# Kernel optimization log

Measured on AMD Instinct MI355X. Metric: run time of the kernel, lower is better.

The kernel has to match this reference:

```python
import jax, jax.numpy as jnp
import numpy as np

B, N, D, H, L = 16, 512, 256, 8, 4
DK = D // H
EPS_LN = 1e-6
EPS_ADJ = 1e-6
NEG_INF = -1e12
LAM_ATT, LAM_DIST, LAM_ADJ = 0.3, 0.3, 0.4
SLOPE = 0.1  # leaky_relu_slope


def setup_inputs() -> dict:
    key = jax.random.key(0)
    ks = jax.random.split(key, 24)
    s = 1.0 / np.sqrt(D)
    w = lambda k: jax.random.normal(k, (L, D, D), jnp.float32) * s
    b = lambda k: jax.random.normal(k, (L, D), jnp.float32) * 0.01
    return {
        "x": jax.random.normal(ks[0], (B, N, D), jnp.float32),
        "mask": jax.random.randint(ks[1], (B, N), 0, 2, jnp.int32),
        "adj_matrix": jax.random.uniform(ks[2], (B, N, N), jnp.float32),
        "distance_matrix": jax.random.uniform(ks[3], (B, N, N), jnp.float32) * 10.0,
        "edges_att": jnp.zeros((1,), jnp.float32),  # unused (use_edge_features=False)
        "Wq": w(ks[4]), "bq": b(ks[5]),
        "Wk": w(ks[6]), "bk": b(ks[7]),
        "Wv": w(ks[8]), "bv": b(ks[9]),
        "Wo": w(ks[10]), "bo": b(ks[11]),
        "Wf1": w(ks[12]), "bf1": b(ks[13]),
        "Wf2": w(ks[14]), "bf2": b(ks[15]),
        "ln1_a": jnp.ones((L, D), jnp.float32), "ln1_b": jnp.zeros((L, D), jnp.float32),
        "ln2_a": jnp.ones((L, D), jnp.float32), "ln2_b": jnp.zeros((L, D), jnp.float32),
        "lnf_a": jnp.ones((D,), jnp.float32), "lnf_b": jnp.zeros((D,), jnp.float32),
    }


def _layernorm(x, a, b):
    # torch LayerNorm here uses unbiased std and divides by (std + eps)
    m = x.mean(-1, keepdims=True)
    s = jnp.std(x, axis=-1, ddof=1, keepdims=True)
    return a * (x - m) / (s + EPS_LN) + b


def reference(x, mask, adj_matrix, distance_matrix, edges_att,
              Wq, bq, Wk, bk, Wv, bv, Wo, bo, Wf1, bf1, Wf2, bf2,
              ln1_a, ln1_b, ln2_a, ln2_b, lnf_a, lnf_b):
    maskk = (mask != 0)[:, None, :]                      # [B,1,N] key mask
    # distance kernel: softmax(-dist) with masked keys -> weight 0
    p_dist = jax.nn.softmax(jnp.where(maskk, -distance_matrix, -jnp.inf), axis=-1)  # [B,N,N]
    # row-normalized adjacency
    p_adj = adj_matrix / (adj_matrix.sum(-1, keepdims=True) + EPS_ADJ)              # [B,N,N]
    mk4 = maskk[:, :, None, :]                           # [B,1,1,N]
    inv_sqrt_dk = 1.0 / np.sqrt(DK)

    for i in range(L):
        # --- self-attention sublayer (pre-norm residual) ---
        h_in = _layernorm(x, ln1_a[i], ln1_b[i])
        q = (h_in @ Wq[i] + bq[i]).reshape(B, N, H, DK).transpose(0, 2, 1, 3)
        k = (h_in @ Wk[i] + bk[i]).reshape(B, N, H, DK).transpose(0, 2, 1, 3)
        v = (h_in @ Wv[i] + bv[i]).reshape(B, N, H, DK).transpose(0, 2, 1, 3)
        scores = jnp.einsum('bhqd,bhkd->bhqk', q, k) * inv_sqrt_dk
        p_attn = jax.nn.softmax(jnp.where(mk4, scores, NEG_INF), axis=-1)
        # three-way fused weighting over [B,H,N,N]
        p = LAM_ATT * p_attn + LAM_DIST * p_dist[:, None] + LAM_ADJ * p_adj[:, None]
        att = jnp.einsum('bhqk,bhkd->bhqd', p, v).transpose(0, 2, 1, 3).reshape(B, N, D)
        x = x + (att @ Wo[i] + bo[i])
        # --- FFN sublayer (pre-norm residual), N_dense=2 with leaky_relu ---
        h2 = _layernorm(x, ln2_a[i], ln2_b[i])
        h2 = jax.nn.leaky_relu(h2 @ Wf1[i] + bf1[i], negative_slope=SLOPE)
        h2 = jax.nn.leaky_relu(h2 @ Wf2[i] + bf2[i], negative_slope=SLOPE)
        x = x + h2

    return _layernorm(x, lnf_a, lnf_b)
```

## Files before the change

### kernel.cpp

```cpp
#include <hip/hip_runtime.h>
#include <hip/hip_bf16.h>
#include <math.h>

constexpr int kB  = 16;
constexpr int kN  = 512;
constexpr int kD  = 256;
constexpr int kH  = 8;
constexpr int kDK = 32;
constexpr int kL  = 4;

using bf16 = __hip_bfloat16;
using short8 = __attribute__((ext_vector_type(8))) short;
using floatx4 = __attribute__((ext_vector_type(4))) float;

__device__ __forceinline__ float fast_exp2(float x) {
#if __has_builtin(__builtin_amdgcn_exp2f)
    return __builtin_amdgcn_exp2f(x);
#else
    return __expf(x * 0.69314718055994531f);
#endif
}

__device__ __forceinline__ float bfs2f(short s) {
    unsigned u = ((unsigned)(unsigned short)s) << 16;
    return __uint_as_float(u);
}

__device__ __forceinline__ void gl2lds16(const bf16* g, bf16* s) {
    __builtin_amdgcn_global_load_lds(
        (const __attribute__((address_space(1))) void*)g,
        (__attribute__((address_space(3))) void*)s, 16, 0, 0);
}

__device__ __forceinline__ int swzA(int row, int inrow_byte) {
    return row * 512 + (inrow_byte ^ ((row & 7) << 4));
}

__device__ __forceinline__ float blockReduceSum(float v, float* sh) {
    #pragma unroll
    for (int o = 32; o > 0; o >>= 1) v += __shfl_down(v, o, 64);
    int lane = threadIdx.x & 63, w = threadIdx.x >> 6;
    __syncthreads();
    if (lane == 0) sh[w] = v;
    __syncthreads();
    return sh[0] + sh[1] + sh[2] + sh[3];
}

__device__ __forceinline__ float blockReduceMax(float v, float* sh) {
    #pragma unroll
    for (int o = 32; o > 0; o >>= 1) v = fmaxf(v, __shfl_down(v, o, 64));
    int lane = threadIdx.x & 63, w = threadIdx.x >> 6;
    __syncthreads();
    if (lane == 0) sh[w] = v;
    __syncthreads();
    return fmaxf(fmaxf(sh[0], sh[1]), fmaxf(sh[2], sh[3]));
}

__global__ __launch_bounds__(256) void wconv_kernel(const float* __restrict__ Wq,
                                                    const float* __restrict__ Wk,
                                                    const float* __restrict__ Wv,
                                                    const float* __restrict__ Wo,
                                                    const float* __restrict__ Wf1,
                                                    const float* __restrict__ Wf2,
                                                    bf16* __restrict__ wqkv,
                                                    bf16* __restrict__ wo,
                                                    bf16* __restrict__ wf1,
                                                    bf16* __restrict__ wf2) {
    __shared__ float tile[32][33];
    int bid = blockIdx.x;
    int mat = bid >> 6;
    int t6 = bid & 63;
    int tr = t6 >> 3, tc = t6 & 7;
    int layer = mat / 6, slot = mat % 6;
    const float* src =
        slot == 0 ? Wq : slot == 1 ? Wk : slot == 2 ? Wv :
        slot == 3 ? Wo : slot == 4 ? Wf1 : Wf2;
    src += (size_t)layer * kD * kD;
    bf16* dst;
    if (slot < 3) dst = wqkv + ((size_t)layer * 768 + slot * 256) * kD;
    else dst = (slot == 3 ? wo : slot == 4 ? wf1 : wf2) + (size_t)layer * kD * kD;
    int t = threadIdx.x;
    int r = t >> 5, c = t & 31;
    #pragma unroll
    for (int i = 0; i < 4; i++)
        tile[r + i * 8][c] = src[(size_t)(tr * 32 + r + i * 8) * kD + tc * 32 + c];
    __syncthreads();
    #pragma unroll
    for (int i = 0; i < 4; i++)
        dst[(size_t)(tc * 32 + r + i * 8) * kD + tr * 32 + c] = bf16(tile[c][r + i * 8]);
}

__global__ __launch_bounds__(256) void bcat_kernel(const float* __restrict__ bq,
                                                   const float* __restrict__ bk,
                                                   const float* __restrict__ bv,
                                                   float* __restrict__ bcat) {
    int idx = blockIdx.x * 256 + threadIdx.x;
    int layer = idx / 768, j = idx % 768;
    const float* s = j < 256 ? bq : j < 512 ? bk : bv;
    bcat[idx] = s[layer * 256 + (j & 255)];
}

__global__ __launch_bounds__(256) void pc_kernel(const float* __restrict__ adj,
                                                 const float* __restrict__ dist,
                                                 const int* __restrict__ mask,
                                                 bf16* __restrict__ pcb) {
    __shared__ float sh[4];
    int row = blockIdx.x;
    int b = row >> 9;
    int t = threadIdx.x;
    const float* dr = dist + (size_t)row * kN;
    const float* ar = adj + (size_t)row * kN;
    const int* mr = mask + b * kN;
    float d0 = dr[t], d1 = dr[t + 256];
    float a0 = ar[t], a1 = ar[t + 256];
    int m0 = mr[t], m1 = mr[t + 256];
    const float kLog2e = 1.4426950408889634f;
    float s0 = m0 ? -d0 * kLog2e : -INFINITY;
    float s1 = m1 ? -d1 * kLog2e : -INFINITY;
    float mx = blockReduceMax(fmaxf(s0, s1), sh);
    float e0 = fast_exp2(s0 - mx);
    float e1 = fast_exp2(s1 - mx);
    float sum  = blockReduceSum(e0 + e1, sh);
    float asum = blockReduceSum(a0 + a1, sh);
    float w_d = 0.3f / sum;
    float w_a = 0.4f / (asum + 1e-6f);
    bf16* pr = pcb + (size_t)row * kN;
    pr[t]       = bf16(e0 * w_d + a0 * w_a);
    pr[t + 256] = bf16(e1 * w_d + a1 * w_a);
}

__global__ __launch_bounds__(256) void ln_kernel(const float* __restrict__ x,
                                                 const float* __restrict__ ga,
                                                 const float* __restrict__ gb,
                                                 bf16* __restrict__ y) {
    __shared__ float sh[4];
    int row = blockIdx.x, t = threadIdx.x;
    float v = x[(size_t)row * kD + t];
    float m = blockReduceSum(v, sh) * (1.0f / kD);
    float dd = v - m;
    float var = blockReduceSum(dd * dd, sh) * (1.0f / (kD - 1));
    float s = sqrtf(var);
    y[(size_t)row * kD + t] = bf16(ga[t] * dd / (s + 1e-6f) + gb[t]);
}

__global__ __launch_bounds__(256) void gemm_qkv(const bf16* __restrict__ A,
                                                const bf16* __restrict__ Wt,
                                                const float* __restrict__ bias,
                                                bf16* __restrict__ Cv) {
    __shared__ __align__(16) bf16 As[2][128][32];
    __shared__ __align__(16) bf16 Bs[2][64][32];
    int t = threadIdx.x;
    int m0 = blockIdx.x * 128, n0 = blockIdx.y * 64;
    int lane = t & 63, w = t >> 6, g = lane >> 4, li = lane & 15;
    int sr = lane >> 2;
    int sc = (lane & 3) * 8;

    const bf16* aSrc0 = A + (size_t)(m0 + w * 32 + sr) * kD + sc;
    const bf16* aSrc1 = aSrc0 + (size_t)16 * kD;
    const bf16* bSrc  = Wt + (size_t)(n0 + w * 16 + sr) * kD + sc;

    floatx4 zero = {0.f, 0.f, 0.f, 0.f};
    floatx4 acc[2][4];
    #pragma unroll
    for (int i = 0; i < 2; i++)
        #pragma unroll
        for (int j = 0; j < 4; j++) acc[i][j] = zero;

    auto stage = [&](int buf, int k0) {
        gl2lds16(aSrc0 + k0, &As[buf][w * 32][0]);
        gl2lds16(aSrc1 + k0, &As[buf][w * 32 + 16][0]);
        gl2lds16(bSrc  + k0, &Bs[buf][w * 16][0]);
    };

    stage(0, 0);
    __syncthreads();

    #pragma unroll
    for (int ks = 0; ks < 8; ks++) {
        const int cur = ks & 1;
        if (ks < 7) stage(cur ^ 1, (ks + 1) * 32);
        short8 af0 = *(const short8*)&As[cur][w * 32 + li][g * 8];
        short8 af1 = *(const short8*)&As[cur][w * 32 + 16 + li][g * 8];
        #pragma unroll
        for (int ct = 0; ct < 4; ct++) {
            short8 bfr = *(const short8*)&Bs[cur][ct * 16 + li][g * 8];
            acc[0][ct] = __builtin_amdgcn_mfma_f32_16x16x32_bf16(af0, bfr, acc[0][ct], 0, 0, 0);
            acc[1][ct] = __builtin_amdgcn_mfma_f32_16x16x32_bf16(af1, bfr, acc[1][ct], 0, 0, 0);
        }
        if (ks < 7) __syncthreads();
    }

    #pragma unroll
    for (int rt = 0; rt < 2; rt++) {
        #pragma unroll
        for (int ct = 0; ct < 4; ct++) {
            #pragma unroll
            for (int rr = 0; rr < 4; rr++) {
                int m = m0 + w * 32 + rt * 16 + g * 4 + rr;
                int n = n0 + ct * 16 + li;
                float v = acc[rt][ct][rr] + bias[n];
                int j = n >> 8, nn = n & 255;
                int b = m >> 9, nr = m & 511;
                int hh = nn >> 5, dk = nn & 31;
                Cv[(size_t)j * (kB * kN * kD) +
                   (((size_t)(b * kH + hh)) * kN + nr) * kDK + dk] = bf16(v);
            }
        }
    }
}

__global__ __launch_bounds__(256, 2) void attn_mfma(const bf16* __restrict__ qb,
                                                    const bf16* __restrict__ kb,
                                                    const bf16* __restrict__ vb,
                                                    const bf16* __restrict__ pcb,
                                                    const int* __restrict__ mask,
                                                    bf16* __restrict__ att) {
    __shared__ __align__(16) bf16 Vf[16 * 2 * 64 * 8];
    __shared__ __align__(16) bf16 Pbuf[4][16][136];

    int blk = blockIdx.x;
    int qt = blk & 7;
    int bh = blk >> 3;
    int b = bh >> 3;
    int h = bh & 7;
    int t = threadIdx.x;
    int lane = t & 63, w = t >> 6;
    int g = lane >> 4, li = lane & 15;

    {
        const float4* vsrc4 = (const float4*)(vb + (size_t)bh * kN * kDK);
        #pragma unroll
        for (int it = 0; it < 8; it++) {
            int idx = t + it * 256;
            float4 raw = vsrc4[idx];
            union { float4 f; bf16 hh[8]; } u; u.f = raw;
            int f0 = idx * 8;
            int n = f0 >> 5, dk0 = f0 & 31;
            int kt = n >> 5, j = n & 7, gsl = (n >> 3) & 3;
            #pragma unroll
            for (int e = 0; e < 8; e++) {
                int dk = dk0 + e;
                int dt = dk >> 4;
                int lsl = (gsl << 4) | (dk & 15);
                Vf[((((kt << 1) | dt) << 6) | lsl) * 8 + j] = u.hh[e];
            }
        }
    }
    __syncthreads();

    const bf16* qrow = qb + ((size_t)bh * kN + qt * 64 + w * 16 + li) * kDK + g * 8;
    short8 aQ = *(const short8*)qrow;
    const bf16* kbase = kb + (size_t)bh * kN * kDK;
    const int* mb = mask + b * kN;
    unsigned mbits = 0;
    #pragma unroll
    for (int tt = 0; tt < 32; tt++)
        mbits |= (unsigned)(mb[tt * 16 + li] != 0) << tt;

    floatx4 s[32];
    floatx4 zero = {0.f, 0.f, 0.f, 0.f};
    #pragma unroll
    for (int tt = 0; tt < 32; tt++) {
        short8 bK = *(const short8*)(kbase + (size_t)(tt * 16 + li) * kDK + g * 8);
        s[tt] = __builtin_amdgcn_mfma_f32_16x16x32_bf16(aQ, bK, zero, 0, 0, 0);
    }

    const float scale = 0.17677669529663689f * 1.4426950408889634f;
    #pragma unroll
    for (int tt = 0; tt < 32; tt++) {
        bool mm = (mbits >> tt) & 1;
        #pragma unroll
        for (int r = 0; r < 4; r++)
            s[tt][r] = mm ? s[tt][r] * scale : -1e12f;
    }

    #pragma unroll
    for (int r = 0; r < 4; r++) {
        float mx = s[0][r];
        #pragma unroll
        for (int tt = 1; tt < 32; tt++) mx = fmaxf(mx, s[tt][r]);
        #pragma unroll
        for (int o = 1; o < 16; o <<= 1) mx = fmaxf(mx, __shfl_xor(mx, o, 64));
        float sum = 0.f;
        #pragma unroll
        for (int tt = 0; tt < 32; tt++) {
            float e = fast_exp2(s[tt][r] - mx);
            s[tt][r] = e;
            sum += e;
        }
        #pragma unroll
        for (int o = 1; o < 16; o <<= 1) sum += __shfl_xor(sum, o, 64);
        float inv = 0.3f / sum;
        #pragma unroll
        for (int tt = 0; tt < 32; tt++) s[tt][r] *= inv;
    }

    {
        const short* pcq = (const short*)(pcb + ((size_t)b * kN + qt * 64 + w * 16) * kN);
        #pragma unroll
        for (int tt = 0; tt < 32; tt++) {
            #pragma unroll
            for (int r = 0; r < 4; r++)
                s[tt][r] += bfs2f(pcq[(size_t)(g * 4 + r) * kN + tt * 16 + li]);
        }
    }

    bf16* pb = &Pbuf[w][0][0];
    floatx4 accA0 = zero, accA1 = zero;
    #pragma unroll
    for (int c = 0; c < 4; c++) {
        #pragma unroll
        for (int ttl = 0; ttl < 8; ttl++) {
            int tt = c * 8 + ttl;
            int kcol = ttl * 16 + li;
            #pragma unroll
            for (int r = 0; r < 4; r++)
                pb[(g * 4 + r) * 136 + kcol] = bf16(s[tt][r]);
        }
        #pragma unroll
        for (int k2 = 0; k2 < 4; k2++) {
            int ktile = c * 4 + k2;
            short8 aP  = *(const short8*)(pb + li * 136 + k2 * 32 + g * 8);
            short8 bV0 = *(const short8*)(&Vf[((ktile * 2 + 0) * 64 + lane) * 8]);
            short8 bV1 = *(const short8*)(&Vf[((ktile * 2 + 1) * 64 + lane) * 8]);
            accA0 = __builtin_amdgcn_mfma_f32_16x16x32_bf16(aP, bV0, accA0, 0, 0, 0);
            accA1 = __builtin_amdgcn_mfma_f32_16x16x32_bf16(aP, bV1, accA1, 0, 0, 0);
        }
    }

    #pragma unroll
    for (int r = 0; r < 4; r++) {
        size_t row = (size_t)b * kN + qt * 64 + w * 16 + g * 4 + r;
        bf16* arow = att + row * kD + h * kDK;
        arow[li]      = bf16(accA0[r]);
        arow[16 + li] = bf16(accA1[r]);
    }
}

__device__ __forceinline__ void gemm_phase32(const char* asb, const bf16* __restrict__ Wt,
                                             bf16 (*Bs)[256][32],
                                             int w, int lane, int g, int li,
                                             floatx4 acc[2][4]) {
    auto stageB = [&](int buf, int k0) {
        #pragma unroll
        for (int c = 0; c < 4; c++) {
            int row = w * 64 + c * 16;
            gl2lds16(Wt + (size_t)(row + (lane >> 2)) * kD + k0 + (lane & 3) * 8,
                     &Bs[buf][row][0]);
        }
    };
    stageB(0, 0);
    __syncthreads();
    #pragma unroll
    for (int ks = 0; ks < 8; ks++) {
        const int cur = ks & 1;
        if (ks < 7) stageB(cur ^ 1, (ks + 1) * 32);
        short8 af0 = *(const short8*)(asb + swzA(li,      (ks * 4 + g) << 4));
        short8 af1 = *(const short8*)(asb + swzA(li + 16, (ks * 4 + g) << 4));
        #pragma unroll
        for (int ct = 0; ct < 4; ct++) {
            short8 bfr = *(const short8*)&Bs[cur][w * 64 + ct * 16 + li][g * 8];
            acc[0][ct] = __builtin_amdgcn_mfma_f32_16x16x32_bf16(af0, bfr, acc[0][ct], 0, 0, 0);
            acc[1][ct] = __builtin_amdgcn_mfma_f32_16x16x32_bf16(af1, bfr, acc[1][ct], 0, 0, 0);
        }
        if (ks < 7) __syncthreads();
    }
}

__device__ __forceinline__ void row_ln_stats(floatx4 xv[2][4],
                                             float (*psumS)[32], float (*psqS)[32],
                                             int w, int g, int li,
                                             float outMean[2][4], float outInv[2][4]) {
    #pragma unroll
    for (int rt = 0; rt < 2; rt++) {
        #pragma unroll
        for (int rr = 0; rr < 4; rr++) {
            float s4 = 0.f, q4 = 0.f;
            #pragma unroll
            for (int ct = 0; ct < 4; ct++) {
                float v = xv[rt][ct][rr];
                s4 += v;
                q4 += v * v;
            }
            #pragma unroll
            for (int o = 1; o < 16; o <<= 1) {
                s4 += __shfl_xor(s4, o, 64);
                q4 += __shfl_xor(q4, o, 64);
            }
            int row = rt * 16 + g * 4 + rr;
            if (li == 0) { psumS[w][row] = s4; psqS[w][row] = q4; }
        }
    }
    __syncthreads();
    #pragma unroll
    for (int rt = 0; rt < 2; rt++) {
        #pragma unroll
        for (int rr = 0; rr < 4; rr++) {
            int row = rt * 16 + g * 4 + rr;
            float s  = psumS[0][row] + psumS[1][row] + psumS[2][row] + psumS[3][row];
            float ss = psqS[0][row]  + psqS[1][row]  + psqS[2][row]  + psqS[3][row];
            float mean = s * (1.0f / kD);
            float var = (ss - (float)kD * mean * mean) * (1.0f / (kD - 1));
            outMean[rt][rr] = mean;
            outInv[rt][rr] = 1.0f / (sqrtf(var) + 1e-6f);
        }
    }
}

template <bool LAST>
__global__ __launch_bounds__(256) void block_tail(const bf16* __restrict__ A,
                                                  const bf16* __restrict__ Wot,
                                                  const float* __restrict__ bo,
                                                  const float* __restrict__ resid,
                                                  const bf16* __restrict__ W1t,
                                                  const float* __restrict__ b1,
                                                  const bf16* __restrict__ W2t,
                                                  const float* __restrict__ b2,
                                                  const float* __restrict__ ln2a,
                                                  const float* __restrict__ ln2b,
                                                  const float* __restrict__ lnna,
                                                  const float* __restrict__ lnnb,
                                                  float* __restrict__ xcOut,
                                                  bf16* __restrict__ hOut,
                                                  float* __restrict__ fOut) {
    __shared__ __align__(16) bf16 As[32][256];
    __shared__ __align__(16) bf16 As2[32][256];
    __shared__ __align__(16) bf16 Bs[2][256][32];
    __shared__ float psumS[4][32], psqS[4][32];

    int t = threadIdx.x;
    int m0 = blockIdx.x * 32;
    int lane = t & 63, w = t >> 6, g = lane >> 4, li = lane & 15;

    {
        int r = t >> 3;
        int cbase = (t & 7) * 4;
        const bf16* src = A + (size_t)(m0 + r) * kD;
        char* asb = (char*)&As[0][0];
        #pragma unroll
        for (int c = 0; c < 4; c++) {
            int chunk = cbase + c;
            short8 v = *(const short8*)(src + chunk * 8);
            *(short8*)(asb + swzA(r, chunk << 4)) = v;
        }
    }

    floatx4 zero = {0.f, 0.f, 0.f, 0.f};
    floatx4 acc[2][4];
    #pragma unroll
    for (int i = 0; i < 2; i++)
        #pragma unroll
        for (int j = 0; j < 4; j++) acc[i][j] = zero;

    gemm_phase32((const char*)&As[0][0], Wot, Bs, w, lane, g, li, acc);

    floatx4 xs[2][4];
    #pragma unroll
    for (int rt = 0; rt < 2; rt++) {
        #pragma unroll
        for (int ct = 0; ct < 4; ct++) {
            #pragma unroll
            for (int rr = 0; rr < 4; rr++) {
                int m = m0 + rt * 16 + g * 4 + rr;
                int n = w * 64 + ct * 16 + li;
                float xv = resid[(size_t)m * kD + n] + acc[rt][ct][rr] + bo[n];
                xs[rt][ct][rr] = xv;
                acc[rt][ct][rr] = xv;
            }
        }
    }

    float mean[2][4], inv[2][4];
    row_ln_stats(acc, psumS, psqS, w, g, li, mean, inv);
    {
        char* asb = (char*)&As[0][0];
        #pragma unroll
        for (int rt = 0; rt < 2; rt++) {
            #pragma unroll
            for (int ct = 0; ct < 4; ct++) {
                #pragma unroll
                for (int rr = 0; rr < 4; rr++) {
                    int row = rt * 16 + g * 4 + rr;
                    int col = w * 64 + ct * 16 + li;
                    float y = ln2a[col] * (xs[rt][ct][rr] - mean[rt][rr]) * inv[rt][rr] + ln2b[col];
                    *(bf16*)(asb + swzA(row, col * 2)) = bf16(y);
                }
            }
        }
    }
    __syncthreads();

    #pragma unroll
    for (int i = 0; i < 2; i++)
        #pragma unroll
        for (int j = 0; j < 4; j++) acc[i][j] = zero;

    gemm_phase32((const char*)&As[0][0], W1t, Bs, w, lane, g, li, acc);

    {
        char* as2b = (char*)&As2[0][0];
        #pragma unroll
        for (int rt = 0; rt < 2; rt++) {
            #pragma unroll
            for (int ct = 0; ct < 4; ct++) {
                #pragma unroll
                for (int rr = 0; rr < 4; rr++) {
                    int row = rt * 16 + g * 4 + rr;
                    int col = w * 64 + ct * 16 + li;
                    float v = acc[rt][ct][rr] + b1[col];
                    v = v > 0.f ? v : 0.1f * v;
                    *(bf16*)(as2b + swzA(row, col * 2)) = bf16(v);
                }
            }
        }
    }
    __syncthreads();

    #pragma unroll
    for (int i = 0; i < 2; i++)
        #pragma unroll
        for (int j = 0; j < 4; j++) acc[i][j] = zero;

    gemm_phase32((const char*)&As2[0][0], W2t, Bs, w, lane, g, li, acc);

    #pragma unroll
    for (int rt = 0; rt < 2; rt++) {
        #pragma unroll
        for (int ct = 0; ct < 4; ct++) {
            #pragma unroll
            for (int rr = 0; rr < 4; rr++) {
                int m = m0 + rt * 16 + g * 4 + rr;
                int n = w * 64 + ct * 16 + li;
                float v = acc[rt][ct][rr] + b2[n];
                v = v > 0.f ? v : 0.1f * v;
                float xv = xs[rt][ct][rr] + v;
                if (!LAST) xcOut[(size_t)m * kD + n] = xv;
                acc[rt][ct][rr] = xv;
            }
        }
    }

    row_ln_stats(acc, psumS, psqS, w, g, li, mean, inv);

    #pragma unroll
    for (int rt = 0; rt < 2; rt++) {
        #pragma unroll
        for (int ct = 0; ct < 4; ct++) {
            #pragma unroll
            for (int rr = 0; rr < 4; rr++) {
                int m = m0 + rt * 16 + g * 4 + rr;
                int n = w * 64 + ct * 16 + li;
                float y = lnna[n] * (acc[rt][ct][rr] - mean[rt][rr]) * inv[rt][rr] + lnnb[n];
                if (LAST) fOut[(size_t)m * kD + n] = y;
                else      hOut[(size_t)m * kD + n] = bf16(y);
            }
        }
    }
}

extern "C" void kernel_launch(void* const* d_in, const int* in_sizes, int n_in,
                              void* d_out, int out_size, void* d_ws, size_t ws_size,
                              hipStream_t stream) {
    const float* x    = (const float*)d_in[0];
    const int*   mask = (const int*)d_in[1];
    const float* adj  = (const float*)d_in[2];
    const float* dist = (const float*)d_in[3];
    const float* Wq = (const float*)d_in[5];  const float* bq = (const float*)d_in[6];
    const float* Wk = (const float*)d_in[7];  const float* bk = (const float*)d_in[8];
    const float* Wv = (const float*)d_in[9];  const float* bv = (const float*)d_in[10];
    const float* Wo = (const float*)d_in[11]; const float* bo = (const float*)d_in[12];
    const float* Wf1 = (const float*)d_in[13]; const float* bf1 = (const float*)d_in[14];
    const float* Wf2 = (const float*)d_in[15]; const float* bf2 = (const float*)d_in[16];
    const float* ln1a = (const float*)d_in[17]; const float* ln1b = (const float*)d_in[18];
    const float* ln2a = (const float*)d_in[19]; const float* ln2b = (const float*)d_in[20];
    const float* lnfa = (const float*)d_in[21]; const float* lnfb = (const float*)d_in[22];

    const size_t rows = (size_t)kB * kN;
    const size_t actN = rows * kD;

    char* wsb = (char*)d_ws;
    bf16*  pcb   = (bf16*)wsb;  wsb += (size_t)kB * kN * kN * sizeof(bf16);
    float* xc    = (float*)wsb; wsb += actN * sizeof(float);
    bf16*  h     = (bf16*)wsb;  wsb += actN * sizeof(bf16);
    bf16*  attb  = (bf16*)wsb;  wsb += actN * sizeof(bf16);
    bf16*  qkvb  = (bf16*)wsb;  wsb += 3 * actN * sizeof(bf16);
    bf16*  wqkv  = (bf16*)wsb;  wsb += (size_t)kL * 768 * kD * sizeof(bf16);
    bf16*  wo_t  = (bf16*)wsb;  wsb += (size_t)kL * kD * kD * sizeof(bf16);
    bf16*  wf1_t = (bf16*)wsb;  wsb += (size_t)kL * kD * kD * sizeof(bf16);
    bf16*  wf2_t = (bf16*)wsb;  wsb += (size_t)kL * kD * kD * sizeof(bf16);
    float* bcat  = (float*)wsb; wsb += (size_t)kL * 768 * sizeof(float);

    wconv_kernel<<<24 * 64, 256, 0, stream>>>(Wq, Wk, Wv, Wo, Wf1, Wf2, wqkv, wo_t, wf1_t, wf2_t);
    bcat_kernel<<<kL * 768 / 256, 256, 0, stream>>>(bq, bk, bv, bcat);
    pc_kernel<<<kB * kN, 256, 0, stream>>>(adj, dist, mask, pcb);
    ln_kernel<<<rows, 256, 0, stream>>>(x, ln1a, ln1b, h);

    dim3 gQKV(64, 12);
    const int g32 = rows / 32;
    for (int i = 0; i < kL; i++) {
        const size_t bOff = (size_t)i * kD;
        const size_t wOff = (size_t)i * kD * kD;
        const float* xin = (i == 0) ? x : xc;
        gemm_qkv<<<gQKV, 256, 0, stream>>>(h, wqkv + (size_t)i * 768 * kD,
                                           bcat + (size_t)i * 768, qkvb);
        attn_mfma<<<kB * kH * (kN / 64), 256, 0, stream>>>(qkvb, qkvb + actN,
                                                           qkvb + 2 * actN,
                                                           pcb, mask, attb);
        if (i < kL - 1) {
            block_tail<false><<<g32, 256, 0, stream>>>(
                attb, wo_t + wOff, bo + bOff, xin,
                wf1_t + wOff, bf1 + bOff, wf2_t + wOff, bf2 + bOff,
                ln2a + bOff, ln2b + bOff,
                ln1a + (size_t)(i + 1) * kD, ln1b + (size_t)(i + 1) * kD,
                xc, h, nullptr);
        } else {
            block_tail<true><<<g32, 256, 0, stream>>>(
                attb, wo_t + wOff, bo + bOff, xin,
                wf1_t + wOff, bf1 + bOff, wf2_t + wOff, bf2 + bOff,
                ln2a + bOff, ln2b + bOff, lnfa, lnfb,
                nullptr, nullptr, (float*)d_out);
        }
    }
}
```

Measured before the change: 386.6 us.

## Merge prep kernels into one launch and process two query tiles per attention block

Folds the weight transpose/convert, bias concat, distance/adjacency precompute and first layernorm into a single prep kernel that dispatches on block index, saving three launches. The attention kernel now has each block handle two 64-row query tiles. That halves the grid and reuses the shared-memory V staging and mask bits across both tiles. The cost is fewer blocks (512) to fill the GPU and a longer serial chain per block, which can hurt latency hiding. The merged prep kernel also carries the larger shared tile for every block.

```diff
diff --git a/kernel.cpp b/kernel.cpp
--- a/kernel.cpp
+++ b/kernel.cpp
@@ -56,91 +56,89 @@
     return fmaxf(fmaxf(sh[0], sh[1]), fmaxf(sh[2], sh[3]));
 }
 
-__global__ __launch_bounds__(256) void wconv_kernel(const float* __restrict__ Wq,
-                                                    const float* __restrict__ Wk,
-                                                    const float* __restrict__ Wv,
-                                                    const float* __restrict__ Wo,
-                                                    const float* __restrict__ Wf1,
-                                                    const float* __restrict__ Wf2,
-                                                    bf16* __restrict__ wqkv,
-                                                    bf16* __restrict__ wo,
-                                                    bf16* __restrict__ wf1,
-                                                    bf16* __restrict__ wf2) {
-    __shared__ float tile[32][33];
-    int bid = blockIdx.x;
-    int mat = bid >> 6;
-    int t6 = bid & 63;
-    int tr = t6 >> 3, tc = t6 & 7;
-    int layer = mat / 6, slot = mat % 6;
-    const float* src =
-        slot == 0 ? Wq : slot == 1 ? Wk : slot == 2 ? Wv :
-        slot == 3 ? Wo : slot == 4 ? Wf1 : Wf2;
-    src += (size_t)layer * kD * kD;
-    bf16* dst;
-    if (slot < 3) dst = wqkv + ((size_t)layer * 768 + slot * 256) * kD;
-    else dst = (slot == 3 ? wo : slot == 4 ? wf1 : wf2) + (size_t)layer * kD * kD;
-    int t = threadIdx.x;
-    int r = t >> 5, c = t & 31;
-    #pragma unroll
-    for (int i = 0; i < 4; i++)
-        tile[r + i * 8][c] = src[(size_t)(tr * 32 + r + i * 8) * kD + tc * 32 + c];
-    __syncthreads();
-    #pragma unroll
-    for (int i = 0; i < 4; i++)
-        dst[(size_t)(tc * 32 + r + i * 8) * kD + tr * 32 + c] = bf16(tile[c][r + i * 8]);
-}
-
-__global__ __launch_bounds__(256) void bcat_kernel(const float* __restrict__ bq,
+__global__ __launch_bounds__(256) void prep_kernel(const float* __restrict__ Wq,
+                                                   const float* __restrict__ Wk,
+                                                   const float* __restrict__ Wv,
+                                                   const float* __restrict__ Wo,
+                                                   const float* __restrict__ Wf1,
+                                                   const float* __restrict__ Wf2,
+                                                   const float* __restrict__ bq,
                                                    const float* __restrict__ bk,
                                                    const float* __restrict__ bv,
-                                                   float* __restrict__ bcat) {
-    int idx = blockIdx.x * 256 + threadIdx.x;
-    int layer = idx / 768, j = idx % 768;
-    const float* s = j < 256 ? bq : j < 512 ? bk : bv;
-    bcat[idx] = s[layer * 256 + (j & 255)];
-}
-
-__global__ __launch_bounds__(256) void pc_kernel(const float* __restrict__ adj,
-                                                 const float* __restrict__ dist,
-                                                 const int* __restrict__ mask,
-                                                 bf16* __restrict__ pcb) {
+                                                   const float* __restrict__ adj,
+                                                   const float* __restrict__ dist,
+                                                   const int* __restrict__ mask,
+                                                   const float* __restrict__ x,
+                                                   const float* __restrict__ ln1a,
+                                                   const float* __restrict__ ln1b,
+                                                   bf16* __restrict__ wqkv,
+                                                   bf16* __restrict__ wo,
+                                                   bf16* __restrict__ wf1,
+                                                   bf16* __restrict__ wf2,
+                                                   float* __restrict__ bcat,
+                                                   bf16* __restrict__ pcb,
+                                                   bf16* __restrict__ h) {
+    __shared__ float tile[32][33];
     __shared__ float sh[4];
-    int row = blockIdx.x;
-    int b = row >> 9;
+    int bid = blockIdx.x;
     int t = threadIdx.x;
-    const float* dr = dist + (size_t)row * kN;
-    const float* ar = adj + (size_t)row * kN;
-    const int* mr = mask + b * kN;
-    float d0 = dr[t], d1 = dr[t + 256];
-    float a0 = ar[t], a1 = ar[t + 256];
-    int m0 = mr[t], m1 = mr[t + 256];
-    const float kLog2e = 1.4426950408889634f;
-    float s0 = m0 ? -d0 * kLog2e : -INFINITY;
-    float s1 = m1 ? -d1 * kLog2e : -INFINITY;
-    float mx = blockReduceMax(fmaxf(s0, s1), sh);
-    float e0 = fast_exp2(s0 - mx);
-    float e1 = fast_exp2(s1 - mx);
-    float sum  = blockReduceSum(e0 + e1, sh);
-    float asum = blockReduceSum(a0 + a1, sh);
-    float w_d = 0.3f / sum;
-    float w_a = 0.4f / (asum + 1e-6f);
-    bf16* pr = pcb + (size_t)row * kN;
-    pr[t]       = bf16(e0 * w_d + a0 * w_a);
-    pr[t + 256] = bf16(e1 * w_d + a1 * w_a);
-}
-
-__global__ __launch_bounds__(256) void ln_kernel(const float* __restrict__ x,
-                                                 const float* __restrict__ ga,
-                                                 const float* __restrict__ gb,
-                                                 bf16* __restrict__ y) {
-    __shared__ float sh[4];
-    int row = blockIdx.x, t = threadIdx.x;
-    float v = x[(size_t)row * kD + t];
-    float m = blockReduceSum(v, sh) * (1.0f / kD);
-    float dd = v - m;
-    float var = blockReduceSum(dd * dd, sh) * (1.0f / (kD - 1));
-    float s = sqrtf(var);
-    y[(size_t)row * kD + t] = bf16(ga[t] * dd / (s + 1e-6f) + gb[t]);
+
+    if (bid < 1536) {
+        int mat = bid >> 6;
+        int t6 = bid & 63;
+        int tr = t6 >> 3, tc = t6 & 7;
+        int layer = mat / 6, slot = mat % 6;
+        const float* src =
+            slot == 0 ? Wq : slot == 1 ? Wk : slot == 2 ? Wv :
+            slot == 3 ? Wo : slot == 4 ? Wf1 : Wf2;
+        src += (size_t)layer * kD * kD;
+        bf16* dst;
+        if (slot < 3) dst = wqkv + ((size_t)layer * 768 + slot * 256) * kD;
+        else dst = (slot == 3 ? wo : slot == 4 ? wf1 : wf2) + (size_t)layer * kD * kD;
+        int r = t >> 5, c = t & 31;
+        #pragma unroll
+        for (int i = 0; i < 4; i++)
+            tile[r + i * 8][c] = src[(size_t)(tr * 32 + r + i * 8) * kD + tc * 32 + c];
+        __syncthreads();
+        #pragma unroll
+        for (int i = 0; i < 4; i++)
+            dst[(size_t)(tc * 32 + r + i * 8) * kD + tr * 32 + c] = bf16(tile[c][r + i * 8]);
+    } else if (bid < 1548) {
+        int idx = (bid - 1536) * 256 + t;
+        int layer = idx / 768, j = idx % 768;
+        const float* s = j < 256 ? bq : j < 512 ? bk : bv;
+        bcat[idx] = s[layer * 256 + (j & 255)];
+    } else if (bid < 1548 + kB * kN) {
+        int row = bid - 1548;
+        int b = row >> 9;
+        const float* dr = dist + (size_t)row * kN;
+        const float* ar = adj + (size_t)row * kN;
+        const int* mr = mask + b * kN;
+        float d0 = dr[t], d1 = dr[t + 256];
+        float a0 = ar[t], a1 = ar[t + 256];
+        int m0 = mr[t], m1 = mr[t + 256];
+        const float kLog2e = 1.4426950408889634f;
+        float s0 = m0 ? -d0 * kLog2e : -INFINITY;
+        float s1 = m1 ? -d1 * kLog2e : -INFINITY;
+        float mx = blockReduceMax(fmaxf(s0, s1), sh);
+        float e0 = fast_exp2(s0 - mx);
+        float e1 = fast_exp2(s1 - mx);
+        float sum  = blockReduceSum(e0 + e1, sh);
+        float asum = blockReduceSum(a0 + a1, sh);
+        float w_d = 0.3f / sum;
+        float w_a = 0.4f / (asum + 1e-6f);
+        bf16* pr = pcb + (size_t)row * kN;
+        pr[t]       = bf16(e0 * w_d + a0 * w_a);
+        pr[t + 256] = bf16(e1 * w_d + a1 * w_a);
+    } else {
+        int row = bid - (1548 + kB * kN);
+        float v = x[(size_t)row * kD + t];
+        float m = blockReduceSum(v, sh) * (1.0f / kD);
+        float dd = v - m;
+        float var = blockReduceSum(dd * dd, sh) * (1.0f / (kD - 1));
+        float s = sqrtf(var);
+        h[(size_t)row * kD + t] = bf16(ln1a[t] * dd / (s + 1e-6f) + ln1b[t]);
+    }
 }
 
 __global__ __launch_bounds__(256) void gemm_qkv(const bf16* __restrict__ A,
@@ -219,13 +217,14 @@
     __shared__ __align__(16) bf16 Pbuf[4][16][136];
 
     int blk = blockIdx.x;
-    int qt = blk & 7;
-    int bh = blk >> 3;
+    int qpair = blk & 3;
+    int bh = blk >> 2;
     int b = bh >> 3;
     int h = bh & 7;
     int t = threadIdx.x;
     int lane = t & 63, w = t >> 6;
     int g = lane >> 4, li = lane & 15;
+    floatx4 zero = {0.f, 0.f, 0.f, 0.f};
 
     {
         const float4* vsrc4 = (const float4*)(vb + (size_t)bh * kN * kDK);
@@ -248,92 +247,97 @@
     }
     __syncthreads();
 
-    const bf16* qrow = qb + ((size_t)bh * kN + qt * 64 + w * 16 + li) * kDK + g * 8;
-    short8 aQ = *(const short8*)qrow;
-    const bf16* kbase = kb + (size_t)bh * kN * kDK;
     const int* mb = mask + b * kN;
     unsigned mbits = 0;
     #pragma unroll
     for (int tt = 0; tt < 32; tt++)
         mbits |= (unsigned)(mb[tt * 16 + li] != 0) << tt;
 
-    floatx4 s[32];
-    floatx4 zero = {0.f, 0.f, 0.f, 0.f};
-    #pragma unroll
-    for (int tt = 0; tt < 32; tt++) {
-        short8 bK = *(const short8*)(kbase + (size_t)(tt * 16 + li) * kDK + g * 8);
-        s[tt] = __builtin_amdgcn_mfma_f32_16x16x32_bf16(aQ, bK, zero, 0, 0, 0);
-    }
-
+    const bf16* kbase = kb + (size_t)bh * kN * kDK;
     const float scale = 0.17677669529663689f * 1.4426950408889634f;
-    #pragma unroll
-    for (int tt = 0; tt < 32; tt++) {
-        bool mm = (mbits >> tt) & 1;
-        #pragma unroll
-        for (int r = 0; r < 4; r++)
-            s[tt][r] = mm ? s[tt][r] * scale : -1e12f;
-    }
-
-    #pragma unroll
-    for (int r = 0; r < 4; r++) {
-        float mx = s[0][r];
-        #pragma unroll
-        for (int tt = 1; tt < 32; tt++) mx = fmaxf(mx, s[tt][r]);
-        #pragma unroll
-        for (int o = 1; o < 16; o <<= 1) mx = fmaxf(mx, __shfl_xor(mx, o, 64));
-        float sum = 0.f;
+    bf16* pb = &Pbuf[w][0][0];
+
+    for (int itq = 0; itq < 2; itq++) {
+        int qt = qpair * 2 + itq;
+
+        const bf16* qrow = qb + ((size_t)bh * kN + qt * 64 + w * 16 + li) * kDK + g * 8;
+        short8 aQ = *(const short8*)qrow;
+
+        floatx4 s[32];
         #pragma unroll
         for (int tt = 0; tt < 32; tt++) {
-            float e = fast_exp2(s[tt][r] - mx);
-            s[tt][r] = e;
-            sum += e;
-        }
-        #pragma unroll
-        for (int o = 1; o < 16; o <<= 1) sum += __shfl_xor(sum, o, 64);
-        float inv = 0.3f / sum;
-        #pragma unroll
-        for (int tt = 0; tt < 32; tt++) s[tt][r] *= inv;
-    }
-
-    {
-        const short* pcq = (const short*)(pcb + ((size_t)b * kN + qt * 64 + w * 16) * kN);
+            short8 bK = *(const short8*)(kbase + (size_t)(tt * 16 + li) * kDK + g * 8);
+            s[tt] = __builtin_amdgcn_mfma_f32_16x16x32_bf16(aQ, bK, zero, 0, 0, 0);
+        }
+
         #pragma unroll
         for (int tt = 0; tt < 32; tt++) {
+            bool mm = (mbits >> tt) & 1;
             #pragma unroll
             for (int r = 0; r < 4; r++)
-                s[tt][r] += bfs2f(pcq[(size_t)(g * 4 + r) * kN + tt * 16 + li]);
-        }
-    }
-
-    bf16* pb = &Pbuf[w][0][0];
-    floatx4 accA0 = zero, accA1 = zero;
-    #pragma unroll
-    for (int c = 0; c < 4; c++) {
-        #pragma unroll
-        for (int ttl = 0; ttl < 8; ttl++) {
-            int tt = c * 8 + ttl;
-            int kcol = ttl * 16 + li;
-            #pragma unroll
-            for (int r = 0; r < 4; r++)
-                pb[(g * 4 + r) * 136 + kcol] = bf16(s[tt][r]);
-        }
-        #pragma unroll
-        for (int k2 = 0; k2 < 4; k2++) {
-            int ktile = c * 4 + k2;
-            short8 aP  = *(const short8*)(pb + li * 136 + k2 * 32 + g * 8);
-            short8 bV0 = *(const short8*)(&Vf[((ktile * 2 + 0) * 64 + lane) * 8]);
-            short8 bV1 = *(const short8*)(&Vf[((ktile * 2 + 1) * 64 + lane) * 8]);
-            accA0 = __builtin_amdgcn_mfma_f32_16x16x32_bf16(aP, bV0, accA0, 0, 0, 0);
-            accA1 = __builtin_amdgcn_mfma_f32_16x16x32_bf16(aP, bV1, accA1, 0, 0, 0);
-        }
-    }
-
-    #pragma unroll
-    for (int r = 0; r < 4; r++) {
-        size_t row = (size_t)b * kN + qt * 64 + w * 16 + g * 4 + r;
-        bf16* arow = att + row * kD + h * kDK;
-        arow[li]      = bf16(accA0[r]);
-        arow[16 + li] = bf16(accA1[r]);
+                s[tt][r] = mm ? s[tt][r] * scale : -1e12f;
+        }
+
+        #pragma unroll
+        for (int r = 0; r < 4; r++) {
+            float mx = s[0][r];
+            #pragma unroll
+            for (int tt = 1; tt < 32; tt++) mx = fmaxf(mx, s[tt][r]);
+            #pragma unroll
+            for (int o = 1; o < 16; o <<= 1) mx = fmaxf(mx, __shfl_xor(mx, o, 64));
+            float sum = 0.f;
+            #pragma unroll
+            for (int tt = 0; tt < 32; tt++) {
+                float e = fast_exp2(s[tt][r] - mx);
+                s[tt][r] = e;
+                sum += e;
+            }
+            #pragma unroll
+            for (int o = 1; o < 16; o <<= 1) sum += __shfl_xor(sum, o, 64);
+            float inv = 0.3f / sum;
+            #pragma unroll
+            for (int tt = 0; tt < 32; tt++) s[tt][r] *= inv;
+        }
+
+        {
+            const short* pcq = (const short*)(pcb + ((size_t)b * kN + qt * 64 + w * 16) * kN);
+            #pragma unroll
+            for (int tt = 0; tt < 32; tt++) {
+                #pragma unroll
+                for (int r = 0; r < 4; r++)
+                    s[tt][r] += bfs2f(pcq[(size_t)(g * 4 + r) * kN + tt * 16 + li]);
+            }
+        }
+
+        floatx4 accA0 = zero, accA1 = zero;
+        #pragma unroll
+        for (int c = 0; c < 4; c++) {
+            #pragma unroll
+            for (int ttl = 0; ttl < 8; ttl++) {
+                int tt = c * 8 + ttl;
+                int kcol = ttl * 16 + li;
+                #pragma unroll
+                for (int r = 0; r < 4; r++)
+                    pb[(g * 4 + r) * 136 + kcol] = bf16(s[tt][r]);
+            }
+            #pragma unroll
+            for (int k2 = 0; k2 < 4; k2++) {
+                int ktile = c * 4 + k2;
+                short8 aP  = *(const short8*)(pb + li * 136 + k2 * 32 + g * 8);
+                short8 bV0 = *(const short8*)(&Vf[((ktile * 2 + 0) * 64 + lane) * 8]);
+                short8 bV1 = *(const short8*)(&Vf[((ktile * 2 + 1) * 64 + lane) * 8]);
+                accA0 = __builtin_amdgcn_mfma_f32_16x16x32_bf16(aP, bV0, accA0, 0, 0, 0);
+                accA1 = __builtin_amdgcn_mfma_f32_16x16x32_bf16(aP, bV1, accA1, 0, 0, 0);
+            }
+        }
+
+        #pragma unroll
+        for (int r = 0; r < 4; r++) {
+            size_t row = (size_t)b * kN + qt * 64 + w * 16 + g * 4 + r;
+            bf16* arow = att + row * kD + h * kDK;
+            arow[li]      = bf16(accA0[r]);
+            arow[16 + li] = bf16(accA1[r]);
+        }
     }
 }
 
@@ -590,10 +594,9 @@
     bf16*  wf2_t = (bf16*)wsb;  wsb += (size_t)kL * kD * kD * sizeof(bf16);
     float* bcat  = (float*)wsb; wsb += (size_t)kL * 768 * sizeof(float);
 
-    wconv_kernel<<<24 * 64, 256, 0, stream>>>(Wq, Wk, Wv, Wo, Wf1, Wf2, wqkv, wo_t, wf1_t, wf2_t);
-    bcat_kernel<<<kL * 768 / 256, 256, 0, stream>>>(bq, bk, bv, bcat);
-    pc_kernel<<<kB * kN, 256, 0, stream>>>(adj, dist, mask, pcb);
-    ln_kernel<<<rows, 256, 0, stream>>>(x, ln1a, ln1b, h);
+    prep_kernel<<<1548 + 2 * kB * kN, 256, 0, stream>>>(
+        Wq, Wk, Wv, Wo, Wf1, Wf2, bq, bk, bv, adj, dist, mask, x, ln1a, ln1b,
+        wqkv, wo_t, wf1_t, wf2_t, bcat, pcb, h);
 
     dim3 gQKV(64, 12);
     const int g32 = rows / 32;
@@ -603,9 +606,9 @@
         const float* xin = (i == 0) ? x : xc;
         gemm_qkv<<<gQKV, 256, 0, stream>>>(h, wqkv + (size_t)i * 768 * kD,
                                            bcat + (size_t)i * 768, qkvb);
-        attn_mfma<<<kB * kH * (kN / 64), 256, 0, stream>>>(qkvb, qkvb + actN,
-                                                           qkvb + 2 * actN,
-                                                           pcb, mask, attb);
+        attn_mfma<<<kB * kH * 4, 256, 0, stream>>>(qkvb, qkvb + actN,
+                                                   qkvb + 2 * actN,
+                                                   pcb, mask, attb);
         if (i < kL - 1) {
             block_tail<false><<<g32, 256, 0, stream>>>(
                 attb, wo_t + wOff, bo + bOff, xin,
```

Result: slower. 562.7 us (+45.6%).
